# Optimization experiments

Hardware: AMD Instinct MI355X
Metric: run time of the kernel (lower is better)

## Reference

```python
import jax, jax.numpy as jnp
import numpy as np

EMBED_DIM = 768
NUM_HEADS = 12
HEAD_DIM = EMBED_DIM // NUM_HEADS


def setup_inputs() -> dict:
    key = jax.random.key(0)
    k1, k2, k3, k4 = jax.random.split(key, 4)
    B, N, D = 8, 1024, EMBED_DIM
    x = jax.random.normal(k1, (B, N, D), dtype=jnp.float32)
    # qkv Linear (no bias): torch weight [3D, D]; we store transposed [D, 3D]
    W_qkv = jax.random.normal(k2, (D, 3 * D), dtype=jnp.float32) * (D ** -0.5)
    # projection Linear with bias
    W_proj = jax.random.normal(k3, (D, D), dtype=jnp.float32) * (D ** -0.5)
    b_proj = jax.random.normal(k4, (D,), dtype=jnp.float32) * 0.01
    return {"x": x, "W_qkv": W_qkv, "W_proj": W_proj, "b_proj": b_proj}


def reference(x, W_qkv, W_proj, b_proj):
    B, N, D = x.shape
    h, d = NUM_HEADS, HEAD_DIM
    scaling = d ** -0.5
    qkv = x @ W_qkv  # [B, N, 3D]
    # 'b n (qkv h d) -> qkv b h n d'
    qkv = qkv.reshape(B, N, 3, h, d).transpose(2, 0, 3, 1, 4)
    q, k, v = qkv[0], qkv[1], qkv[2]  # each [B, h, N, d]
    energy = jnp.einsum('bhid,bhjd->bhij', q, k) * scaling  # [B, h, N, N]
    att = jax.nn.softmax(energy, axis=-1)
    out = jnp.einsum('bhij,bhjd->bhid', att, v)  # [B, h, N, d]
    out = out.transpose(0, 2, 1, 3).reshape(B, N, D)  # 'b h n d -> b n (h d)'
    out = out @ W_proj + b_proj
    return out
```

## Files before the change

kernel.cpp:

```cpp
#include <hip/hip_runtime.h>
#include <hip/hip_bf16.h>

#define NUM_B 8
#define SEQ   1024
#define DIM   768
#define NH    12
#define HD    64

typedef __bf16 bf16x8 __attribute__((ext_vector_type(8)));
typedef float  f32x4  __attribute__((ext_vector_type(4)));
typedef unsigned int u32;

#define QSCL 0.18033688011112042f

__device__ __forceinline__ unsigned short f2bf(float f) {
  unsigned int u = __float_as_uint(f);
  u += 0x7FFFu + ((u >> 16) & 1u);
  return (unsigned short)(u >> 16);
}

__device__ __forceinline__ float fexp2(float x) { return __builtin_exp2f(x); }

__device__ __forceinline__ void gload_lds16(const void* g, void* l) {
  __builtin_amdgcn_global_load_lds(
      (const __attribute__((address_space(1))) unsigned int*)g,
      (__attribute__((address_space(3))) unsigned int*)l, 16, 0, 0);
}

__global__ void cvt_kernel(const float* __restrict__ in, unsigned short* __restrict__ out, int n) {
  int i = (blockIdx.x * blockDim.x + threadIdx.x) * 4;
  if (i >= n) return;
  float4 v = *(const float4*)(in + i);
  ushort4 o = { f2bf(v.x), f2bf(v.y), f2bf(v.z), f2bf(v.w) };
  *(ushort4*)(out + i) = o;
}

__global__ void tcvt_kernel(const float* __restrict__ in, unsigned short* __restrict__ out,
                            int R, int C) {
  __shared__ unsigned short tile[32][33];
  int c0 = blockIdx.x * 32, r0 = blockIdx.y * 32;
  int tx = threadIdx.x, ty = threadIdx.y;
  #pragma unroll
  for (int i = 0; i < 32; i += 8)
    tile[ty + i][tx] = f2bf(in[(size_t)(r0 + ty + i) * C + c0 + tx]);
  __syncthreads();
  #pragma unroll
  for (int i = 0; i < 32; i += 8)
    out[(size_t)(c0 + ty + i) * R + r0 + tx] = tile[tx][ty + i];
}

template<bool QKV>
__global__ __launch_bounds__(256) void gemm_bf16(
    const unsigned short* __restrict__ A,
    const unsigned short* __restrict__ Bt,
    int K,
    unsigned short* __restrict__ qb,
    unsigned short* __restrict__ kb,
    unsigned short* __restrict__ vt,
    float* __restrict__ outp,
    const float* __restrict__ bias)
{
  __shared__ short As[128 * 32];
  __shared__ short Bs[128 * 32];
  const int m0 = blockIdx.x * 128, n0 = blockIdx.y * 128;
  const int t = threadIdx.x;
  const int lane = t & 63, w = t >> 6;
  const int l15 = lane & 15, g = lane >> 4;
  const int wm = w >> 1, wn = w & 1;

  const int ch0 = t, ch1 = t + 256;
  const size_t szK = (size_t)K;
  const unsigned short* Ag0 = A  + (size_t)(m0 + (ch0 >> 2)) * szK + (ch0 & 3) * 8;
  const unsigned short* Ag1 = A  + (size_t)(m0 + (ch1 >> 2)) * szK + (ch1 & 3) * 8;
  const unsigned short* Bg0 = Bt + (size_t)(n0 + (ch0 >> 2)) * szK + (ch0 & 3) * 8;
  const unsigned short* Bg1 = Bt + (size_t)(n0 + (ch1 >> 2)) * szK + (ch1 & 3) * 8;
  short* Al0 = &As[w * 512];
  short* Al1 = Al0 + 2048;
  short* Bl0 = &Bs[w * 512];
  short* Bl1 = Bl0 + 2048;

  f32x4 zv = {0.f, 0.f, 0.f, 0.f};
  f32x4 acc[4][4];
  #pragma unroll
  for (int i = 0; i < 4; ++i)
    #pragma unroll
    for (int j = 0; j < 4; ++j) acc[i][j] = zv;

  for (int k0 = 0; k0 < K; k0 += 32) {
    __syncthreads();
    gload_lds16(Ag0 + k0, Al0);
    gload_lds16(Ag1 + k0, Al1);
    gload_lds16(Bg0 + k0, Bl0);
    gload_lds16(Bg1 + k0, Bl1);
    asm volatile("s_waitcnt vmcnt(0)" ::: "memory");
    __syncthreads();
    bf16x8 af[4], bfr[4];
    #pragma unroll
    for (int i = 0; i < 4; ++i) af[i]  = *(const bf16x8*)&As[(wm*64 + i*16 + l15) * 32 + g*8];
    #pragma unroll
    for (int i = 0; i < 4; ++i) bfr[i] = *(const bf16x8*)&Bs[(wn*64 + i*16 + l15) * 32 + g*8];
    #pragma unroll
    for (int i = 0; i < 4; ++i)
      #pragma unroll
      for (int j = 0; j < 4; ++j)
        acc[i][j] = __builtin_amdgcn_mfma_f32_16x16x32_bf16(af[i], bfr[j], acc[i][j], 0, 0, 0);
  }

  const int mbase = m0 + wm * 64, nbase = n0 + wn * 64;
  if (QKV) {
    #pragma unroll
    for (int i = 0; i < 4; ++i) {
      #pragma unroll
      for (int j = 0; j < 4; ++j) {
        int n = nbase + j * 16 + l15;
        int which = n / DIM;
        int jr = n - which * DIM;
        int head = jr >> 6, dd = jr & 63;
        float sc = (which == 0) ? QSCL : 1.0f;
        #pragma unroll
        for (int r = 0; r < 4; ++r) {
          int m = mbase + i * 16 + g * 4 + r;
          int bb = m >> 10, nn = m & 1023;
          unsigned short val = f2bf(acc[i][j][r] * sc);
          size_t bh = (size_t)bb * NH + head;
          if (which == 0)      qb[(bh * SEQ + nn) * HD + dd] = val;
          else if (which == 1) kb[(bh * SEQ + nn) * HD + dd] = val;
          else {
            int nnp = (nn & ~31) | ((nn & 12) << 1) | ((nn & 16) >> 2) | (nn & 3);
            vt[(bh * HD + dd) * SEQ + nnp] = val;
          }
        }
      }
    }
  } else {
    #pragma unroll
    for (int i = 0; i < 4; ++i)
      #pragma unroll
      for (int j = 0; j < 4; ++j) {
        int n = nbase + j * 16 + l15;
        float bv = bias[n];
        #pragma unroll
        for (int r = 0; r < 4; ++r) {
          int m = mbase + i * 16 + g * 4 + r;
          outp[(size_t)m * DIM + n] = acc[i][j][r] + bv;
        }
      }
  }
}

__global__ __launch_bounds__(256) void attn_kernel(
    const unsigned short* __restrict__ qb,
    const unsigned short* __restrict__ kb,
    const unsigned short* __restrict__ vt,
    unsigned short* __restrict__ ao)
{
  __shared__ short lds[2][2][4096];
  const int bid = blockIdx.x;
  const int qt = (bid & 7) * 128;
  const int bh = bid >> 3;
  const int t = threadIdx.x, lane = t & 63, w = t >> 6;
  const int l15 = lane & 15, g = lane >> 4;
  const unsigned short* Qp = qb + (size_t)bh * SEQ * HD;
  const unsigned short* Kp = kb + (size_t)bh * SEQ * HD;
  const unsigned short* Vp = vt + (size_t)bh * HD * SEQ;
  const int q0 = qt + w * 32;
  const int swz = l15 & 7;

  int offK[2], offV[2], ldso[2];
  #pragma unroll
  for (int i = 0; i < 2; ++i) {
    int chunk = ((w * 2 + i) << 6) + lane;
    int row = chunk >> 3;
    int c = (chunk & 7) ^ (row & 7);
    offK[i] = row * HD + c * 8;
    offV[i] = row * SEQ + c * 8;
    ldso[i] = (w * 2 + i) << 9;
  }

  bf16x8 bq[2][2];
  #pragma unroll
  for (int nq = 0; nq < 2; ++nq)
    #pragma unroll
    for (int kk = 0; kk < 2; ++kk)
      bq[nq][kk] = *(const bf16x8*)(Qp + (size_t)(q0 + nq*16 + l15) * HD + kk*32 + g*8);

  bf16x8 ones;
  #pragma unroll
  for (int i = 0; i < 8; ++i) ones[i] = (__bf16)1.0f;

  f32x4 zv = {0.f, 0.f, 0.f, 0.f};
  f32x4 accO[2][4];
  f32x4 rsac[2] = { zv, zv };
  float m_[2] = { -INFINITY, -INFINITY };
  #pragma unroll
  for (int nq = 0; nq < 2; ++nq)
    #pragma unroll
    for (int fn = 0; fn < 4; ++fn) accO[nq][fn] = zv;

  #pragma unroll
  for (int i = 0; i < 2; ++i) {
    gload_lds16(Kp + offK[i], &lds[0][0][ldso[i]]);
    gload_lds16(Vp + offV[i], &lds[0][1][ldso[i]]);
  }
  asm volatile("s_waitcnt vmcnt(0)" ::: "memory");
  __syncthreads();

  int cur = 0;
  for (int kt = 0; kt < SEQ; kt += 64) {
    if (kt + 64 < SEQ) {
      #pragma unroll
      for (int i = 0; i < 2; ++i) {
        gload_lds16(Kp + (size_t)(kt + 64) * HD + offK[i], &lds[cur ^ 1][0][ldso[i]]);
        gload_lds16(Vp + (kt + 64) + offV[i], &lds[cur ^ 1][1][ldso[i]]);
      }
    }
    const short* Kb = &lds[cur][0][0];
    const short* Vb = &lds[cur][1][0];

    f32x4 s[2][4];
    #pragma unroll
    for (int nq = 0; nq < 2; ++nq)
      #pragma unroll
      for (int fm = 0; fm < 4; ++fm) s[nq][fm] = zv;
    #pragma unroll
    for (int fm = 0; fm < 4; ++fm)
      #pragma unroll
      for (int kk = 0; kk < 2; ++kk) {
        bf16x8 ak = *(const bf16x8*)&Kb[(fm*16 + l15) * 64 + (((kk*4 + g) ^ swz) << 3)];
        s[0][fm] = __builtin_amdgcn_mfma_f32_16x16x32_bf16(ak, bq[0][kk], s[0][fm], 0, 0, 0);
        s[1][fm] = __builtin_amdgcn_mfma_f32_16x16x32_bf16(ak, bq[1][kk], s[1][fm], 0, 0, 0);
      }

    bf16x8 av[4][2];
    #pragma unroll
    for (int fn = 0; fn < 4; ++fn)
      #pragma unroll
      for (int cc = 0; cc < 2; ++cc)
        av[fn][cc] = *(const bf16x8*)&Vb[(fn*16 + l15) * 64 + (((cc*4 + g) ^ swz) << 3)];

    bf16x8 pb[2][2];
    #pragma unroll
    for (int nq = 0; nq < 2; ++nq) {
      f32x4 mc;
      #pragma unroll
      for (int r = 0; r < 4; ++r)
        mc[r] = fmaxf(fmaxf(s[nq][0][r], s[nq][1][r]), fmaxf(s[nq][2][r], s[nq][3][r]));
      float mx = fmaxf(fmaxf(mc[0], mc[1]), fmaxf(mc[2], mc[3]));
      mx = fmaxf(mx, __shfl_xor(mx, 16, 64));
      mx = fmaxf(mx, __shfl_xor(mx, 32, 64));
      float mo = m_[nq];
      if (__any(mx > mo + 11.0f)) {
        float mn = fmaxf(mo, mx);
        float al = fexp2(mo - mn);
        m_[nq] = mn;
        rsac[nq] *= al;
        #pragma unroll
        for (int fn = 0; fn < 4; ++fn)
          #pragma unroll
          for (int r = 0; r < 4; ++r) accO[nq][fn][r] *= al;
      }
      float mn = m_[nq];
      #pragma unroll
      for (int cc = 0; cc < 2; ++cc)
        #pragma unroll
        for (int h = 0; h < 2; ++h)
          #pragma unroll
          for (int r = 0; r < 4; ++r)
            pb[nq][cc][h*4 + r] = (__bf16)fexp2(s[nq][2*cc + h][r] - mn);
      rsac[nq] = __builtin_amdgcn_mfma_f32_16x16x32_bf16(ones, pb[nq][0], rsac[nq], 0, 0, 0);
      rsac[nq] = __builtin_amdgcn_mfma_f32_16x16x32_bf16(ones, pb[nq][1], rsac[nq], 0, 0, 0);
    }

    #pragma unroll
    for (int cc = 0; cc < 2; ++cc)
      #pragma unroll
      for (int fn = 0; fn < 4; ++fn) {
        accO[0][fn] = __builtin_amdgcn_mfma_f32_16x16x32_bf16(av[fn][cc], pb[0][cc], accO[0][fn], 0, 0, 0);
        accO[1][fn] = __builtin_amdgcn_mfma_f32_16x16x32_bf16(av[fn][cc], pb[1][cc], accO[1][fn], 0, 0, 0);
      }

    asm volatile("s_waitcnt vmcnt(0)" ::: "memory");
    __syncthreads();
    cur ^= 1;
  }

  const int bb = bh / NH, hh = bh - bb * NH;
  #pragma unroll
  for (int nq = 0; nq < 2; ++nq) {
    float inv = 1.0f / rsac[nq][0];
    int q = q0 + nq * 16 + l15;
    unsigned short* op = ao + ((size_t)(bb * SEQ + q)) * DIM + hh * HD + g * 4;
    #pragma unroll
    for (int fn = 0; fn < 4; ++fn) {
      ushort4 o = { f2bf(accO[nq][fn][0] * inv), f2bf(accO[nq][fn][1] * inv),
                    f2bf(accO[nq][fn][2] * inv), f2bf(accO[nq][fn][3] * inv) };
      *(ushort4*)(op + fn * 16) = o;
    }
  }
}

extern "C" void kernel_launch(void* const* d_in, const int* in_sizes, int n_in,
                              void* d_out, int out_size, void* d_ws, size_t ws_size,
                              hipStream_t stream) {
  const float* x     = (const float*)d_in[0];
  const float* Wqkv  = (const float*)d_in[1];
  const float* Wproj = (const float*)d_in[2];
  const float* bproj = (const float*)d_in[3];
  float* out = (float*)d_out;

  unsigned short* ws = (unsigned short*)d_ws;
  const size_t NX = (size_t)NUM_B * SEQ * DIM;
  unsigned short* x_bf    = ws;
  unsigned short* Wqkv_t  = x_bf + NX;
  unsigned short* Wproj_t = Wqkv_t + (size_t)3 * DIM * DIM;
  unsigned short* qbuf    = Wproj_t + (size_t)DIM * DIM;
  unsigned short* kbuf    = qbuf + NX;
  unsigned short* vtb     = kbuf + NX;
  unsigned short* attb    = vtb + NX;

  cvt_kernel<<<dim3((unsigned)(NX / 4 / 256)), 256, 0, stream>>>(x, x_bf, (int)NX);
  tcvt_kernel<<<dim3(3 * DIM / 32, DIM / 32), dim3(32, 8), 0, stream>>>(Wqkv, Wqkv_t, DIM, 3 * DIM);
  tcvt_kernel<<<dim3(DIM / 32, DIM / 32), dim3(32, 8), 0, stream>>>(Wproj, Wproj_t, DIM, DIM);

  gemm_bf16<true><<<dim3(64, 18), 256, 0, stream>>>(
      x_bf, Wqkv_t, DIM, qbuf, kbuf, vtb, nullptr, nullptr);

  attn_kernel<<<dim3(NUM_B * NH * (SEQ / 128)), 256, 0, stream>>>(qbuf, kbuf, vtb, attb);

  gemm_bf16<false><<<dim3(64, 6), 256, 0, stream>>>(
      attb, Wproj_t, DIM, nullptr, nullptr, nullptr, out, bproj);
}
```

Measured before the change: 224.0 us.

## Double-buffer GEMM LDS tiles and XOR-swizzle shared memory layout

The bf16 GEMM kernel now uses two LDS buffers, issuing the next k-slice's global-to-LDS loads before computing on the current slice so memory latency overlaps the MFMA work. It also applies an XOR swizzle to the 16-byte chunk position within each LDS row, on both the load and the fragment-read sides, to reduce LDS bank conflicts. The cost is doubled LDS usage per block, which may lower occupancy.

Measured after the change: 220.8 us. No clear change (-1.4%).

```diff
diff --git a/kernel.cpp b/kernel.cpp
--- a/kernel.cpp
+++ b/kernel.cpp
@@ -60,24 +60,24 @@
     float* __restrict__ outp,
     const float* __restrict__ bias)
 {
-  __shared__ short As[128 * 32];
-  __shared__ short Bs[128 * 32];
+  __shared__ short As[2][128 * 32];
+  __shared__ short Bs[2][128 * 32];
   const int m0 = blockIdx.x * 128, n0 = blockIdx.y * 128;
   const int t = threadIdx.x;
   const int lane = t & 63, w = t >> 6;
   const int l15 = lane & 15, g = lane >> 4;
   const int wm = w >> 1, wn = w & 1;
+  const int sx = (l15 >> 1) & 3;
 
   const int ch0 = t, ch1 = t + 256;
   const size_t szK = (size_t)K;
-  const unsigned short* Ag0 = A  + (size_t)(m0 + (ch0 >> 2)) * szK + (ch0 & 3) * 8;
-  const unsigned short* Ag1 = A  + (size_t)(m0 + (ch1 >> 2)) * szK + (ch1 & 3) * 8;
-  const unsigned short* Bg0 = Bt + (size_t)(n0 + (ch0 >> 2)) * szK + (ch0 & 3) * 8;
-  const unsigned short* Bg1 = Bt + (size_t)(n0 + (ch1 >> 2)) * szK + (ch1 & 3) * 8;
-  short* Al0 = &As[w * 512];
-  short* Al1 = Al0 + 2048;
-  short* Bl0 = &Bs[w * 512];
-  short* Bl1 = Bl0 + 2048;
+  const int r0c = ch0 >> 2, g0c = (ch0 & 3) ^ ((ch0 >> 3) & 3);
+  const int r1c = ch1 >> 2, g1c = (ch1 & 3) ^ ((ch1 >> 3) & 3);
+  const unsigned short* Ag0 = A  + (size_t)(m0 + r0c) * szK + g0c * 8;
+  const unsigned short* Ag1 = A  + (size_t)(m0 + r1c) * szK + g1c * 8;
+  const unsigned short* Bg0 = Bt + (size_t)(n0 + r0c) * szK + g0c * 8;
+  const unsigned short* Bg1 = Bt + (size_t)(n0 + r1c) * szK + g1c * 8;
+  const int lb0 = w * 512, lb1 = 2048 + w * 512;
 
   f32x4 zv = {0.f, 0.f, 0.f, 0.f};
   f32x4 acc[4][4];
@@ -86,24 +86,36 @@
     #pragma unroll
     for (int j = 0; j < 4; ++j) acc[i][j] = zv;
 
+  gload_lds16(Ag0, &As[0][lb0]);
+  gload_lds16(Ag1, &As[0][lb1]);
+  gload_lds16(Bg0, &Bs[0][lb0]);
+  gload_lds16(Bg1, &Bs[0][lb1]);
+  asm volatile("s_waitcnt vmcnt(0)" ::: "memory");
+  __syncthreads();
+
+  int cur = 0;
   for (int k0 = 0; k0 < K; k0 += 32) {
-    __syncthreads();
-    gload_lds16(Ag0 + k0, Al0);
-    gload_lds16(Ag1 + k0, Al1);
-    gload_lds16(Bg0 + k0, Bl0);
-    gload_lds16(Bg1 + k0, Bl1);
+    if (k0 + 32 < K) {
+      gload_lds16(Ag0 + k0 + 32, &As[cur ^ 1][lb0]);
+      gload_lds16(Ag1 + k0 + 32, &As[cur ^ 1][lb1]);
+      gload_lds16(Bg0 + k0 + 32, &Bs[cur ^ 1][lb0]);
+      gload_lds16(Bg1 + k0 + 32, &Bs[cur ^ 1][lb1]);
+    }
+    bf16x8 af[4], bfr[4];
+    #pragma unroll
+    for (int i = 0; i < 4; ++i)
+      af[i]  = *(const bf16x8*)&As[cur][(wm*64 + i*16 + l15) * 32 + ((g ^ sx) << 3)];
+    #pragma unroll
+    for (int i = 0; i < 4; ++i)
+      bfr[i] = *(const bf16x8*)&Bs[cur][(wn*64 + i*16 + l15) * 32 + ((g ^ sx) << 3)];
+    #pragma unroll
+    for (int i = 0; i < 4; ++i)
+      #pragma unroll
+      for (int j = 0; j < 4; ++j)
+        acc[i][j] = __builtin_amdgcn_mfma_f32_16x16x32_bf16(af[i], bfr[j], acc[i][j], 0, 0, 0);
     asm volatile("s_waitcnt vmcnt(0)" ::: "memory");
     __syncthreads();
-    bf16x8 af[4], bfr[4];
-    #pragma unroll
-    for (int i = 0; i < 4; ++i) af[i]  = *(const bf16x8*)&As[(wm*64 + i*16 + l15) * 32 + g*8];
-    #pragma unroll
-    for (int i = 0; i < 4; ++i) bfr[i] = *(const bf16x8*)&Bs[(wn*64 + i*16 + l15) * 32 + g*8];
-    #pragma unroll
-    for (int i = 0; i < 4; ++i)
-      #pragma unroll
-      for (int j = 0; j < 4; ++j)
-        acc[i][j] = __builtin_amdgcn_mfma_f32_16x16x32_bf16(af[i], bfr[j], acc[i][j], 0, 0, 0);
+    cur ^= 1;
   }
 
   const int mbase = m0 + wm * 64, nbase = n0 + wn * 64;
```
